# Optimization experiments

Measured on AMD Instinct MI355X. Metric: run time of the kernel, lower is better.

## Reference

```python
import jax, jax.numpy as jnp
import numpy as np

TABLE_SZ = 2 ** 14
FEAT_DIM = 2
NUM_LEVELS = 16
MIN_RES = 16.0
MAX_RES = 512.0
B = 1 << 20

# corner order v0..v7 from get_nearest_vertices_coords (z-ascending, ccw)
OFFSETS = jnp.array([[0, 0, 0], [1, 0, 0], [1, 1, 0], [0, 1, 0],
                     [0, 0, 1], [1, 0, 1], [1, 1, 1], [0, 1, 1]], dtype=jnp.int32)


def setup_inputs() -> dict:
    key = jax.random.key(0)
    kx, kt = jax.random.split(key)
    x = jax.random.uniform(kx, (B, 3), dtype=jnp.float32)  # coords in [0,1)
    # RandomUniform(-1e-4, 1e-4) initializer for all 16 tables, stacked
    tables = jax.random.uniform(kt, (NUM_LEVELS, TABLE_SZ, FEAT_DIM),
                                dtype=jnp.float32, minval=-1e-4, maxval=1e-4)
    return {"x": x, "tables": tables}


def reference(x, tables):
    # per-level resolutions: floor(min_res * b**l), b geometric growth factor
    b = jnp.exp((jnp.log(MAX_RES) - jnp.log(MIN_RES)) / (NUM_LEVELS - 1))
    res = jnp.floor(MIN_RES * b ** jnp.arange(NUM_LEVELS, dtype=jnp.float32))  # [L]

    # NOTE: original computes interp weights from the UNSCALED position
    # (position - floor(position)); since x in [0,1) this equals x. Faithful.
    w = x - jnp.floor(x)  # [B,3]
    off = OFFSETS.astype(bool)[None]  # [1,8,3]
    # trilinear weight per corner: prod over xyz of (w if offset else 1-w)
    cw = jnp.prod(jnp.where(off, w[:, None, :], 1.0 - w[:, None, :]), axis=-1)  # [B,8]

    P1 = jnp.uint32(2654435761)
    P2 = jnp.uint32(805459861)
    TS = jnp.uint32(TABLE_SZ)

    def level(carry, lvl):
        table, r = lvl  # [T,F], scalar
        sp = r * x  # [B,3]
        low = jnp.floor(sp).astype(jnp.int32)
        high = jnp.ceil(sp).astype(jnp.int32)
        corners = jnp.where(off, high[:, None, :], low[:, None, :]).astype(jnp.uint32)  # [B,8,3]
        # spatial hash: x ^ (p1*y) ^ (p2*z) mod table_sz (uint32 wraparound;
        # table_sz is a power of two so this matches int32-wrap + floormod)
        h = (corners[..., 0] ^ (P1 * corners[..., 1]) ^ (P2 * corners[..., 2])) % TS
        feats = table[h.astype(jnp.int32)]  # gather -> [B,8,F]
        return carry, jnp.einsum('bkf,bk->bf', feats, cw)  # [B,F]

    _, outs = jax.lax.scan(level, None, (tables, res))  # [L,B,F]
    # matches tf.concat over levels along feature axis
    return jnp.transpose(outs, (1, 0, 2)).reshape(x.shape[0], NUM_LEVELS * FEAT_DIM)
```

## Files before the change

kernel.cpp:

```cpp
#include <hip/hip_runtime.h>
#include <cmath>

#define TABLE_SZ 16384
#define NLEV 16
#define HALF 8

struct ResArr { float r[NLEV]; };

__global__ __launch_bounds__(256) void cvt_tables(
    const float* __restrict__ src, uint32_t* __restrict__ dst, int n_entries)
{
    int i = blockIdx.x * blockDim.x + threadIdx.x;
    int e = i * 4;
    if (e + 3 < n_entries) {
        const float4* s4 = (const float4*)(src) + i * 2;
        float4 a = s4[0], b = s4[1];
        uint32_t o[4];
        float v[8] = {a.x,a.y,a.z,a.w,b.x,b.y,b.z,b.w};
        #pragma unroll
        for (int k = 0; k < 4; ++k) {
            uint32_t lo = __float_as_uint(v[2*k+0]);
            uint32_t hi = __float_as_uint(v[2*k+1]);
            lo = (lo + 0x7FFFu + ((lo >> 16) & 1u)) >> 16;
            hi = (hi + 0x7FFFu + ((hi >> 16) & 1u)) & 0xFFFF0000u;
            o[k] = lo | hi;
        }
        *(uint4*)(dst + e) = make_uint4(o[0], o[1], o[2], o[3]);
    }
}

template <int TBLOCK>
__device__ __forceinline__ void stage_bf(const uint32_t* __restrict__ tb, int l,
                                         uint32_t* buf, int tid, int wid)
{
    const char* gbase = (const char*)tb + (size_t)l * (TABLE_SZ * 4);
    #pragma unroll
    for (int j = 0; j < (TABLE_SZ * 4) / (TBLOCK * 16); ++j) {
        uint32_t goff = (uint32_t)(j * (TBLOCK * 16) + tid * 16);
        uint32_t loff = (uint32_t)(j * (TBLOCK * 16) + wid * 1024);
        __builtin_amdgcn_global_load_lds(
            (const __attribute__((address_space(1))) uint32_t*)(gbase + goff),
            (__attribute__((address_space(3))) uint32_t*)((char*)buf + loff),
            16, 0, 0);
    }
}

__device__ __forceinline__ float2 level_accum_bf(const uint32_t* tab, float r,
                                                 float px, float py, float pz,
                                                 const float* cw)
{
    const uint32_t P1 = 2654435761u, P2 = 805459861u;
    const uint32_t m  = TABLE_SZ - 1u;

    float sx = r*px, sy = r*py, sz = r*pz;
    uint32_t lx = (uint32_t)sx;
    uint32_t hx = (uint32_t)ceilf(sx);
    uint32_t ly = (uint32_t)sy;
    uint32_t hy = (uint32_t)ceilf(sy);
    uint32_t lz = (uint32_t)sz;
    uint32_t hz = (uint32_t)ceilf(sz);
    uint32_t yl = P1*ly, yh = P1*hy;
    uint32_t zl = P2*lz, zh = P2*hz;

    float a0, a1;
    {
        uint32_t v0 = tab[(lx ^ yl ^ zl) & m];
        uint32_t v1 = tab[(hx ^ yl ^ zl) & m];
        uint32_t v2 = tab[(hx ^ yh ^ zl) & m];
        uint32_t v3 = tab[(lx ^ yh ^ zl) & m];
        a0  = __uint_as_float(v0 << 16)         * cw[0];
        a1  = __uint_as_float(v0 & 0xFFFF0000u) * cw[0];
        a0 += __uint_as_float(v1 << 16)         * cw[1];
        a1 += __uint_as_float(v1 & 0xFFFF0000u) * cw[1];
        a0 += __uint_as_float(v2 << 16)         * cw[2];
        a1 += __uint_as_float(v2 & 0xFFFF0000u) * cw[2];
        a0 += __uint_as_float(v3 << 16)         * cw[3];
        a1 += __uint_as_float(v3 & 0xFFFF0000u) * cw[3];
    }
    {
        uint32_t v4 = tab[(lx ^ yl ^ zh) & m];
        uint32_t v5 = tab[(hx ^ yl ^ zh) & m];
        uint32_t v6 = tab[(hx ^ yh ^ zh) & m];
        uint32_t v7 = tab[(lx ^ yh ^ zh) & m];
        a0 += __uint_as_float(v4 << 16)         * cw[4];
        a1 += __uint_as_float(v4 & 0xFFFF0000u) * cw[4];
        a0 += __uint_as_float(v5 << 16)         * cw[5];
        a1 += __uint_as_float(v5 & 0xFFFF0000u) * cw[5];
        a0 += __uint_as_float(v6 << 16)         * cw[6];
        a1 += __uint_as_float(v6 & 0xFFFF0000u) * cw[6];
        a0 += __uint_as_float(v7 << 16)         * cw[7];
        a1 += __uint_as_float(v7 & 0xFFFF0000u) * cw[7];
    }
    return make_float2(a0, a1);
}

template <int TBLOCK, int TPPT>
__global__ __launch_bounds__(TBLOCK) void mrhe_db(
    const float* __restrict__ x,
    const uint32_t* __restrict__ tb,
    float* __restrict__ out,
    ResArr res, int B)
{
    constexpr int ROUNDS = (TABLE_SZ * 4) / (TBLOCK * 16);
    static_assert(ROUNDS == 4 || ROUNDS == 8 || ROUNDS == 16, "vmcnt literal");

    __shared__ uint32_t tab[2][TABLE_SZ];

    const int tid  = threadIdx.x;
    const int wid  = tid >> 6;
    const int base = blockIdx.x * (TBLOCK * TPPT);

    float px[TPPT], py[TPPT], pz[TPPT];
    float cw[TPPT][8];
    #pragma unroll
    for (int p = 0; p < TPPT; ++p) {
        int idx = base + p * TBLOCK + tid;
        size_t j = (idx < B) ? (size_t)idx : 0;
        px[p] = x[3*j+0]; py[p] = x[3*j+1]; pz[p] = x[3*j+2];
        float ax = 1.0f - px[p], ay = 1.0f - py[p], az = 1.0f - pz[p];
        cw[p][0] = (ax*ay)*az;
        cw[p][1] = (px[p]*ay)*az;
        cw[p][2] = (px[p]*py[p])*az;
        cw[p][3] = (ax*py[p])*az;
        cw[p][4] = (ax*ay)*pz[p];
        cw[p][5] = (px[p]*ay)*pz[p];
        cw[p][6] = (px[p]*py[p])*pz[p];
        cw[p][7] = (ax*py[p])*pz[p];
    }

    stage_bf<TBLOCK>(tb, 0, tab[0], tid, wid);

    float o[TPPT][2*HALF];

    #pragma unroll
    for (int l = 0; l < NLEV; ++l) {
        if (l + 1 < NLEV) {
            stage_bf<TBLOCK>(tb, l + 1, tab[(l + 1) & 1], tid, wid);
            if constexpr (ROUNDS == 4)
                asm volatile("s_waitcnt vmcnt(4)" ::: "memory");
            else if constexpr (ROUNDS == 8)
                asm volatile("s_waitcnt vmcnt(8)" ::: "memory");
            else
                asm volatile("s_waitcnt vmcnt(16)" ::: "memory");
        } else {
            asm volatile("s_waitcnt vmcnt(0)" ::: "memory");
        }
        asm volatile("s_barrier" ::: "memory");

        const float r = res.r[l];
        const uint32_t* buf = tab[l & 1];
        #pragma unroll
        for (int p = 0; p < TPPT; ++p) {
            float2 a = level_accum_bf(buf, r, px[p], py[p], pz[p], cw[p]);
            o[p][2*(l & 7) + 0] = a.x;
            o[p][2*(l & 7) + 1] = a.y;
        }

        if ((l & 7) == 7) {
            const int half = l >> 3;
            #pragma unroll
            for (int p = 0; p < TPPT; ++p) {
                int idx = base + p * TBLOCK + tid;
                if (idx < B) {
                    float* po = out + (size_t)idx * (2*NLEV) + half * (2*HALF);
                    #pragma unroll
                    for (int j = 0; j < (2*HALF)/4; ++j) {
                        float4 v;
                        v.x = o[p][4*j+0]; v.y = o[p][4*j+1];
                        v.z = o[p][4*j+2]; v.w = o[p][4*j+3];
                        ((float4*)po)[j] = v;
                    }
                }
            }
        }

        asm volatile("s_barrier" ::: "memory");
    }
}

__global__ __launch_bounds__(256) void mrhe_direct(
    const float* __restrict__ x,
    const float* __restrict__ tables,
    float* __restrict__ out,
    ResArr res, int B)
{
    int i = blockIdx.x * blockDim.x + threadIdx.x;
    if (i >= B) return;
    float px = x[3*(size_t)i+0], py = x[3*(size_t)i+1], pz = x[3*(size_t)i+2];
    float ax = 1.0f - px, ay = 1.0f - py, az = 1.0f - pz;
    float cw[8] = {(ax*ay)*az,(px*ay)*az,(px*py)*az,(ax*py)*az,
                   (ax*ay)*pz,(px*ay)*pz,(px*py)*pz,(ax*py)*pz};
    const uint32_t P1 = 2654435761u, P2 = 805459861u, m = TABLE_SZ - 1u;
    float o[2*NLEV];
    #pragma unroll
    for (int l = 0; l < NLEV; ++l) {
        float r = res.r[l];
        float sx = r*px, sy = r*py, sz = r*pz;
        uint32_t lx = (uint32_t)sx, hx = (uint32_t)ceilf(sx);
        uint32_t ly = (uint32_t)sy, hy = (uint32_t)ceilf(sy);
        uint32_t lz = (uint32_t)sz, hz = (uint32_t)ceilf(sz);
        uint32_t yl = P1*ly, yh = P1*hy, zl = P2*lz, zh = P2*hz;
        uint32_t h[8] = {(lx^yl^zl)&m,(hx^yl^zl)&m,(hx^yh^zl)&m,(lx^yh^zl)&m,
                         (lx^yl^zh)&m,(hx^yl^zh)&m,(hx^yh^zh)&m,(lx^yh^zh)&m};
        const float2* tbl = (const float2*)tables + (size_t)l * TABLE_SZ;
        float a0 = 0.f, a1 = 0.f;
        #pragma unroll
        for (int k = 0; k < 8; ++k) {
            float2 f = tbl[h[k]];
            a0 += f.x * cw[k]; a1 += f.y * cw[k];
        }
        o[2*l+0] = a0; o[2*l+1] = a1;
    }
    float4* po = (float4*)(out + (size_t)i * (2*NLEV));
    #pragma unroll
    for (int j = 0; j < (2*NLEV)/4; ++j) {
        float4 v; v.x = o[4*j+0]; v.y = o[4*j+1]; v.z = o[4*j+2]; v.w = o[4*j+3];
        po[j] = v;
    }
}

extern "C" void kernel_launch(void* const* d_in, const int* in_sizes, int n_in,
                              void* d_out, int out_size, void* d_ws, size_t ws_size,
                              hipStream_t stream)
{
    const float* x      = (const float*)d_in[0];
    const float* tables = (const float*)d_in[1];
    float* out = (float*)d_out;
    int B = in_sizes[0] / 3;

    ResArr res;
    float bgrow = expf((logf(512.0f) - logf(16.0f)) / 15.0f);
    for (int l = 0; l < NLEV; ++l)
        res.r[l] = floorf(16.0f * powf(bgrow, (float)l));

    const int n_entries = NLEV * TABLE_SZ;
    const size_t need = (size_t)n_entries * 4;

    if (ws_size >= need && d_ws) {
        uint32_t* tb = (uint32_t*)d_ws;
        hipLaunchKernelGGL(cvt_tables, dim3(n_entries/4/256), dim3(256), 0, stream,
                           tables, tb, n_entries);

        hipFuncAttributes attr{};
        hipError_t e = hipFuncGetAttributes(&attr, (const void*)mrhe_db<1024, 1>);
        bool use1024 = (e == hipSuccess) && (attr.localSizeBytes == 0);

        if (use1024) {
            int per_block = 1024 * 1;
            int grid = (B + per_block - 1) / per_block;
            hipLaunchKernelGGL((mrhe_db<1024, 1>), dim3(grid), dim3(1024), 0, stream,
                               x, tb, out, res, B);
        } else {
            int per_block = 512 * 2;
            int grid = (B + per_block - 1) / per_block;
            hipLaunchKernelGGL((mrhe_db<512, 2>), dim3(grid), dim3(512), 0, stream,
                               x, tb, out, res, B);
        }
    } else {
        int grid = (B + 255) / 256;
        hipLaunchKernelGGL(mrhe_direct, dim3(grid), dim3(256), 0, stream,
                           x, tables, out, res, B);
    }
}
```

Measured before the change: 108.1 us.

## Switch table packing to fp16 and default to 512-thread blocks with two points per thread

The packed table format changes from bf16 to fp16, so conversion uses hardware casts and unpacking becomes fp16-to-float conversions. The hash computation derives the high-corner y and z products from the low ones by conditional addition, saving multiplies. The launcher now prefers the 512x2 configuration, with 256x4 as the fallback, replacing the 1024x1 default. Behaviour with 1024 threads per block versus 512 changes occupancy and barrier cost. fp16 keeps more mantissa than bf16 for these small values, though magnitudes near 1e-4 sit close to the fp16 subnormal range.

```diff
diff --git a/kernel.cpp b/kernel.cpp
--- a/kernel.cpp
+++ b/kernel.cpp
@@ -3,7 +3,6 @@
 
 #define TABLE_SZ 16384
 #define NLEV 16
-#define HALF 8
 
 struct ResArr { float r[NLEV]; };
 
@@ -15,23 +14,21 @@
     if (e + 3 < n_entries) {
         const float4* s4 = (const float4*)(src) + i * 2;
         float4 a = s4[0], b = s4[1];
+        float v[8] = {a.x,a.y,a.z,a.w,b.x,b.y,b.z,b.w};
         uint32_t o[4];
-        float v[8] = {a.x,a.y,a.z,a.w,b.x,b.y,b.z,b.w};
         #pragma unroll
         for (int k = 0; k < 4; ++k) {
-            uint32_t lo = __float_as_uint(v[2*k+0]);
-            uint32_t hi = __float_as_uint(v[2*k+1]);
-            lo = (lo + 0x7FFFu + ((lo >> 16) & 1u)) >> 16;
-            hi = (hi + 0x7FFFu + ((hi >> 16) & 1u)) & 0xFFFF0000u;
-            o[k] = lo | hi;
+            unsigned short lo = __builtin_bit_cast(unsigned short, (_Float16)v[2*k+0]);
+            unsigned short hi = __builtin_bit_cast(unsigned short, (_Float16)v[2*k+1]);
+            o[k] = (uint32_t)lo | ((uint32_t)hi << 16);
         }
         *(uint4*)(dst + e) = make_uint4(o[0], o[1], o[2], o[3]);
     }
 }
 
 template <int TBLOCK>
-__device__ __forceinline__ void stage_bf(const uint32_t* __restrict__ tb, int l,
-                                         uint32_t* buf, int tid, int wid)
+__device__ __forceinline__ void stage_h(const uint32_t* __restrict__ tb, int l,
+                                        uint32_t* buf, int tid, int wid)
 {
     const char* gbase = (const char*)tb + (size_t)l * (TABLE_SZ * 4);
     #pragma unroll
@@ -45,51 +42,42 @@
     }
 }
 
-__device__ __forceinline__ float2 level_accum_bf(const uint32_t* tab, float r,
-                                                 float px, float py, float pz,
-                                                 const float* cw)
+__device__ __forceinline__ float2 level_accum_h(const uint32_t* tab, float r,
+                                                float px, float py, float pz,
+                                                const float* cw)
 {
     const uint32_t P1 = 2654435761u, P2 = 805459861u;
     const uint32_t m  = TABLE_SZ - 1u;
 
     float sx = r*px, sy = r*py, sz = r*pz;
-    uint32_t lx = (uint32_t)sx;
-    uint32_t hx = (uint32_t)ceilf(sx);
-    uint32_t ly = (uint32_t)sy;
-    uint32_t hy = (uint32_t)ceilf(sy);
-    uint32_t lz = (uint32_t)sz;
-    uint32_t hz = (uint32_t)ceilf(sz);
-    uint32_t yl = P1*ly, yh = P1*hy;
-    uint32_t zl = P2*lz, zh = P2*hz;
-
-    float a0, a1;
-    {
-        uint32_t v0 = tab[(lx ^ yl ^ zl) & m];
-        uint32_t v1 = tab[(hx ^ yl ^ zl) & m];
-        uint32_t v2 = tab[(hx ^ yh ^ zl) & m];
-        uint32_t v3 = tab[(lx ^ yh ^ zl) & m];
-        a0  = __uint_as_float(v0 << 16)         * cw[0];
-        a1  = __uint_as_float(v0 & 0xFFFF0000u) * cw[0];
-        a0 += __uint_as_float(v1 << 16)         * cw[1];
-        a1 += __uint_as_float(v1 & 0xFFFF0000u) * cw[1];
-        a0 += __uint_as_float(v2 << 16)         * cw[2];
-        a1 += __uint_as_float(v2 & 0xFFFF0000u) * cw[2];
-        a0 += __uint_as_float(v3 << 16)         * cw[3];
-        a1 += __uint_as_float(v3 & 0xFFFF0000u) * cw[3];
-    }
-    {
-        uint32_t v4 = tab[(lx ^ yl ^ zh) & m];
-        uint32_t v5 = tab[(hx ^ yl ^ zh) & m];
-        uint32_t v6 = tab[(hx ^ yh ^ zh) & m];
-        uint32_t v7 = tab[(lx ^ yh ^ zh) & m];
-        a0 += __uint_as_float(v4 << 16)         * cw[4];
-        a1 += __uint_as_float(v4 & 0xFFFF0000u) * cw[4];
-        a0 += __uint_as_float(v5 << 16)         * cw[5];
-        a1 += __uint_as_float(v5 & 0xFFFF0000u) * cw[5];
-        a0 += __uint_as_float(v6 << 16)         * cw[6];
-        a1 += __uint_as_float(v6 & 0xFFFF0000u) * cw[6];
-        a0 += __uint_as_float(v7 << 16)         * cw[7];
-        a1 += __uint_as_float(v7 & 0xFFFF0000u) * cw[7];
+    uint32_t lx = (uint32_t)sx,  hx = (uint32_t)ceilf(sx);
+    uint32_t ly = (uint32_t)sy,  hy = (uint32_t)ceilf(sy);
+    uint32_t lz = (uint32_t)sz,  hz = (uint32_t)ceilf(sz);
+    uint32_t yl = P1*ly;
+    uint32_t yh = (hy == ly) ? yl : yl + P1;
+    uint32_t zl = P2*lz;
+    uint32_t zh = (hz == lz) ? zl : zl + P2;
+
+    uint32_t h0 = (lx ^ yl ^ zl) & m;
+    uint32_t h1 = (hx ^ yl ^ zl) & m;
+    uint32_t h2 = (hx ^ yh ^ zl) & m;
+    uint32_t h3 = (lx ^ yh ^ zl) & m;
+    uint32_t h4 = (lx ^ yl ^ zh) & m;
+    uint32_t h5 = (hx ^ yl ^ zh) & m;
+    uint32_t h6 = (hx ^ yh ^ zh) & m;
+    uint32_t h7 = (lx ^ yh ^ zh) & m;
+
+    uint32_t v0 = tab[h0], v1 = tab[h1], v2 = tab[h2], v3 = tab[h3];
+    uint32_t v4 = tab[h4], v5 = tab[h5], v6 = tab[h6], v7 = tab[h7];
+
+    float a0 = 0.f, a1 = 0.f;
+    uint32_t vv[8] = {v0,v1,v2,v3,v4,v5,v6,v7};
+    #pragma unroll
+    for (int k = 0; k < 8; ++k) {
+        _Float16 lo = __builtin_bit_cast(_Float16, (unsigned short)(vv[k] & 0xFFFFu));
+        _Float16 hi = __builtin_bit_cast(_Float16, (unsigned short)(vv[k] >> 16));
+        a0 += (float)lo * cw[k];
+        a1 += (float)hi * cw[k];
     }
     return make_float2(a0, a1);
 }
@@ -102,7 +90,7 @@
     ResArr res, int B)
 {
     constexpr int ROUNDS = (TABLE_SZ * 4) / (TBLOCK * 16);
-    static_assert(ROUNDS == 4 || ROUNDS == 8 || ROUNDS == 16, "vmcnt literal");
+    static_assert(ROUNDS == 8 || ROUNDS == 16, "vmcnt literal must match");
 
     __shared__ uint32_t tab[2][TABLE_SZ];
 
@@ -118,27 +106,21 @@
         size_t j = (idx < B) ? (size_t)idx : 0;
         px[p] = x[3*j+0]; py[p] = x[3*j+1]; pz[p] = x[3*j+2];
         float ax = 1.0f - px[p], ay = 1.0f - py[p], az = 1.0f - pz[p];
-        cw[p][0] = (ax*ay)*az;
-        cw[p][1] = (px[p]*ay)*az;
-        cw[p][2] = (px[p]*py[p])*az;
-        cw[p][3] = (ax*py[p])*az;
-        cw[p][4] = (ax*ay)*pz[p];
-        cw[p][5] = (px[p]*ay)*pz[p];
-        cw[p][6] = (px[p]*py[p])*pz[p];
-        cw[p][7] = (ax*py[p])*pz[p];
-    }
-
-    stage_bf<TBLOCK>(tb, 0, tab[0], tid, wid);
-
-    float o[TPPT][2*HALF];
+        cw[p][0] = (ax*ay)*az;          cw[p][1] = (px[p]*ay)*az;
+        cw[p][2] = (px[p]*py[p])*az;    cw[p][3] = (ax*py[p])*az;
+        cw[p][4] = (ax*ay)*pz[p];       cw[p][5] = (px[p]*ay)*pz[p];
+        cw[p][6] = (px[p]*py[p])*pz[p]; cw[p][7] = (ax*py[p])*pz[p];
+    }
+
+    stage_h<TBLOCK>(tb, 0, tab[0], tid, wid);
+
+    float o[TPPT][16];
 
     #pragma unroll
     for (int l = 0; l < NLEV; ++l) {
         if (l + 1 < NLEV) {
-            stage_bf<TBLOCK>(tb, l + 1, tab[(l + 1) & 1], tid, wid);
-            if constexpr (ROUNDS == 4)
-                asm volatile("s_waitcnt vmcnt(4)" ::: "memory");
-            else if constexpr (ROUNDS == 8)
+            stage_h<TBLOCK>(tb, l + 1, tab[(l + 1) & 1], tid, wid);
+            if constexpr (ROUNDS == 8)
                 asm volatile("s_waitcnt vmcnt(8)" ::: "memory");
             else
                 asm volatile("s_waitcnt vmcnt(16)" ::: "memory");
@@ -147,11 +129,10 @@
         }
         asm volatile("s_barrier" ::: "memory");
 
-        const float r = res.r[l];
         const uint32_t* buf = tab[l & 1];
         #pragma unroll
         for (int p = 0; p < TPPT; ++p) {
-            float2 a = level_accum_bf(buf, r, px[p], py[p], pz[p], cw[p]);
+            float2 a = level_accum_h(buf, res.r[l], px[p], py[p], pz[p], cw[p]);
             o[p][2*(l & 7) + 0] = a.x;
             o[p][2*(l & 7) + 1] = a.y;
         }
@@ -162,13 +143,13 @@
             for (int p = 0; p < TPPT; ++p) {
                 int idx = base + p * TBLOCK + tid;
                 if (idx < B) {
-                    float* po = out + (size_t)idx * (2*NLEV) + half * (2*HALF);
+                    float* po = out + (size_t)idx * (2*NLEV) + half * 16;
                     #pragma unroll
-                    for (int j = 0; j < (2*HALF)/4; ++j) {
+                    for (int q = 0; q < 4; ++q) {
                         float4 v;
-                        v.x = o[p][4*j+0]; v.y = o[p][4*j+1];
-                        v.z = o[p][4*j+2]; v.w = o[p][4*j+3];
-                        ((float4*)po)[j] = v;
+                        v.x = o[p][4*q+0]; v.y = o[p][4*q+1];
+                        v.z = o[p][4*q+2]; v.w = o[p][4*q+3];
+                        ((float4*)po)[q] = v;
                     }
                 }
             }
@@ -213,9 +194,9 @@
     }
     float4* po = (float4*)(out + (size_t)i * (2*NLEV));
     #pragma unroll
-    for (int j = 0; j < (2*NLEV)/4; ++j) {
-        float4 v; v.x = o[4*j+0]; v.y = o[4*j+1]; v.z = o[4*j+2]; v.w = o[4*j+3];
-        po[j] = v;
+    for (int q = 0; q < (2*NLEV)/4; ++q) {
+        float4 v; v.x = o[4*q+0]; v.y = o[4*q+1]; v.z = o[4*q+2]; v.w = o[4*q+3];
+        po[q] = v;
     }
 }
 
@@ -242,19 +223,19 @@
                            tables, tb, n_entries);
 
         hipFuncAttributes attr{};
-        hipError_t e = hipFuncGetAttributes(&attr, (const void*)mrhe_db<1024, 1>);
-        bool use1024 = (e == hipSuccess) && (attr.localSizeBytes == 0);
-
-        if (use1024) {
-            int per_block = 1024 * 1;
-            int grid = (B + per_block - 1) / per_block;
-            hipLaunchKernelGGL((mrhe_db<1024, 1>), dim3(grid), dim3(1024), 0, stream,
-                               x, tb, out, res, B);
-        } else {
+        hipError_t e = hipFuncGetAttributes(&attr, (const void*)mrhe_db<512, 2>);
+        bool use512 = (e == hipSuccess) && (attr.localSizeBytes == 0);
+
+        if (use512) {
             int per_block = 512 * 2;
             int grid = (B + per_block - 1) / per_block;
             hipLaunchKernelGGL((mrhe_db<512, 2>), dim3(grid), dim3(512), 0, stream,
                                x, tb, out, res, B);
+        } else {
+            int per_block = 256 * 4;
+            int grid = (B + per_block - 1) / per_block;
+            hipLaunchKernelGGL((mrhe_db<256, 4>), dim3(grid), dim3(256), 0, stream,
+                               x, tb, out, res, B);
         }
     } else {
         int grid = (B + 255) / 256;
```

Measured after the change: 109.2 us, median of 2. About the same (+1.0%).
